# Performance work log

Measured on AMD Instinct MI355X. Metric: run time of the kernel, lower is better.

The kernel has to match this reference:

```python
import jax, jax.numpy as jnp
import numpy as np
from jax import lax

SUBSTEPS = 10
MACRO_DT = 1.0
MICRO_DT = MACRO_DT / float(SUBSTEPS)
MAX_DAYS = 4  # matches fill_max of delta_t_days; inactive batch items are masked to zero update


def _laplacian3d(u):
    # u: [B, 1, D, H, W]; 6-point stencil with zero (Dirichlet) padding at the boundary
    up = jnp.pad(u, ((0, 0), (0, 0), (1, 1), (1, 1), (1, 1)))
    return (up[:, :, 2:, 1:-1, 1:-1] + up[:, :, :-2, 1:-1, 1:-1]
            + up[:, :, 1:-1, 2:, 1:-1] + up[:, :, 1:-1, :-2, 1:-1]
            + up[:, :, 1:-1, 1:-1, 2:] + up[:, :, 1:-1, 1:-1, :-2]
            - 6.0 * u)


def _fisher_kolmogorov(u, D_map, rho_map):
    # du/dt = D * laplacian(u) + rho * u * (1 - u)
    return D_map * _laplacian3d(u) + rho_map * u * (1.0 - u)


def setup_inputs() -> dict:
    key = jax.random.key(0)
    k1, k2, k3, k4 = jax.random.split(key, 4)
    shape = (2, 1, 128, 128, 128)
    u_t0 = jax.random.uniform(k1, shape, dtype=jnp.float32)
    D_map = jax.random.uniform(k2, shape, dtype=jnp.float32) * 0.1   # diffusion, keep CFL-stable
    rho_map = jax.random.uniform(k3, shape, dtype=jnp.float32) * 0.5  # proliferation rate
    delta_t_days = jax.random.randint(k4, (2,), 0, MAX_DAYS, dtype=jnp.int32)
    return {"u_t0": u_t0, "D_map": D_map, "rho_map": rho_map, "delta_t_days": delta_t_days}


def reference(u_t0, D_map, rho_map, delta_t_days):
    # Sequential explicit-Euler rollout with per-batch-item active masking.
    days = jnp.arange(MAX_DAYS * SUBSTEPS, dtype=jnp.int32) // SUBSTEPS  # macro day of each micro-step

    def micro_step(u, day):
        active = (day < delta_t_days).astype(u.dtype)[:, None, None, None, None]  # [B,1,1,1,1]
        du_dt = _fisher_kolmogorov(u, D_map, rho_map)
        return u + active * MICRO_DT * du_dt, None

    u_final, _ = lax.scan(micro_step, u_t0, days)
    return jnp.clip(u_final, 0.0, 1.0)
```

## Files before the change

kernel.cpp:

```cpp
#include <hip/hip_runtime.h>


constexpr int NX = 128, NY = 128, NZ = 128;
constexpr int PLANE = NX * NY;
constexpr int VOL   = NZ * PLANE;
constexpr int TOTAL = 2 * VOL;
constexpr int NQ    = TOTAL / 4;
constexpr int ZB    = 4;
constexpr int NTHREADS = NQ / ZB;
constexpr int STEP_BLOCKS = NTHREADS / 256;
constexpr int CLIP_BLOCKS = NQ / 256;
constexpr float DT = 0.1f;
constexpr int MAX_STEPS = 40;

__device__ __forceinline__ float4 ld4(const float* p) {
    return *(const float4*)p;
}

__global__ __launch_bounds__(256)
void fk_step(const float* __restrict__ src, float* __restrict__ dst,
             const float* __restrict__ Dm, const float* __restrict__ Rm,
             const int* __restrict__ dtd, int t)
{
    const int tid = blockIdx.x * 256 + threadIdx.x;
    const int b   = tid >> 17;

    int d = dtd[b];
    d = d < 0 ? 0 : (d > 4 ? 4 : d);
    if (t >= d * 10) return;

    const int xq = tid & 31;
    const int y  = (tid >> 5) & (NY - 1);
    const int zb = (tid >> 12) & 31;
    const int z0 = zb * ZB;
    const int base = (b << 21) + z0 * PLANE + y * NX + (xq << 2);

    const float4 zero = make_float4(0.f, 0.f, 0.f, 0.f);

    float4 up[ZB + 2];
    #pragma unroll
    for (int j = 0; j < ZB + 2; ++j) {
        const int z = z0 - 1 + j;
        up[j] = (z >= 0 && z < NZ) ? ld4(src + base + (j - 1) * PLANE) : zero;
    }

    float4 ym[ZB], yp[ZB], Dv[ZB], Rv[ZB];
    float lft[ZB], rgt[ZB];
    const bool has_ym = (y > 0), has_yp = (y < NY - 1);
    const bool has_l = (xq > 0), has_r = (xq < 31);
    #pragma unroll
    for (int k = 0; k < ZB; ++k) {
        const int idx = base + k * PLANE;
        ym[k] = has_ym ? ld4(src + idx - NX) : zero;
        yp[k] = has_yp ? ld4(src + idx + NX) : zero;
        lft[k] = has_l ? src[idx - 1] : 0.0f;
        rgt[k] = has_r ? src[idx + 4] : 0.0f;
        Dv[k] = ld4(Dm + idx);
        Rv[k] = ld4(Rm + idx);
    }

    #pragma unroll
    for (int k = 0; k < ZB; ++k) {
        const float4 c  = up[k + 1];
        const float4 zm = up[k];
        const float4 zp = up[k + 2];
        float4 o;
        {
            const float lap = (lft[k] + c.y) + (ym[k].x + yp[k].x) + (zm.x + zp.x) - 6.0f * c.x;
            o.x = fmaf(DT, fmaf(Dv[k].x, lap, Rv[k].x * c.x * (1.0f - c.x)), c.x);
        }
        {
            const float lap = (c.x + c.z) + (ym[k].y + yp[k].y) + (zm.y + zp.y) - 6.0f * c.y;
            o.y = fmaf(DT, fmaf(Dv[k].y, lap, Rv[k].y * c.y * (1.0f - c.y)), c.y);
        }
        {
            const float lap = (c.y + c.w) + (ym[k].z + yp[k].z) + (zm.z + zp.z) - 6.0f * c.z;
            o.z = fmaf(DT, fmaf(Dv[k].z, lap, Rv[k].z * c.z * (1.0f - c.z)), c.z);
        }
        {
            const float lap = (c.z + rgt[k]) + (ym[k].w + yp[k].w) + (zm.w + zp.w) - 6.0f * c.w;
            o.w = fmaf(DT, fmaf(Dv[k].w, lap, Rv[k].w * c.w * (1.0f - c.w)), c.w);
        }
        *(float4*)(dst + base + k * PLANE) = o;
    }
}

__global__ __launch_bounds__(256)
void fk_clip(const float* __restrict__ u0, float* __restrict__ out,
             const int* __restrict__ dtd)
{
    const int i4 = blockIdx.x * 256 + threadIdx.x;
    const int b  = i4 >> 19;
    int d = dtd[b];
    d = d < 0 ? 0 : (d > 4 ? 4 : d);
    const float4 v = (d > 0) ? ((const float4*)out)[i4] : ((const float4*)u0)[i4];
    float4 o;
    o.x = fminf(fmaxf(v.x, 0.0f), 1.0f);
    o.y = fminf(fmaxf(v.y, 0.0f), 1.0f);
    o.z = fminf(fmaxf(v.z, 0.0f), 1.0f);
    o.w = fminf(fmaxf(v.w, 0.0f), 1.0f);
    ((float4*)out)[i4] = o;
}

extern "C" void kernel_launch(void* const* d_in, const int* in_sizes, int n_in,
                              void* d_out, int out_size, void* d_ws, size_t ws_size,
                              hipStream_t stream) {
    const float* u0  = (const float*)d_in[0];
    const float* Dm  = (const float*)d_in[1];
    const float* Rm  = (const float*)d_in[2];
    const int*   dtd = (const int*)d_in[3];
    float* out = (float*)d_out;
    float* ws  = (float*)d_ws;

    for (int t = 0; t < MAX_STEPS; ++t) {
        const float* src = (t == 0) ? u0 : ((t & 1) ? ws : out);
        float* dst = (t & 1) ? out : ws;
        fk_step<<<STEP_BLOCKS, 256, 0, stream>>>(src, dst, Dm, Rm, dtd, t);
    }
    fk_clip<<<CLIP_BLOCKS, 256, 0, stream>>>(u0, out, dtd);
}
```

Measured before the change: 286.3 us.

## Pack D and rho maps into bf16 pairs and fold clip into last step

Adds a pre-pass kernel that converts the diffusion and proliferation maps to bf16 and interleaves them into one 32-bit word per voxel. Each step then reads half the coefficient bytes. The separate clip kernel is removed: the clip is applied on each batch item's final step, and items with zero steps copy u0 into the output while clipping. The bf16 coefficients lose precision relative to the fp32 reference, which risks tolerance failures, and the final-step parity must land in the output buffer.

Result: faster. 275.1 us (-3.9%).

```diff
diff --git a/kernel.cpp b/kernel.cpp
--- a/kernel.cpp
+++ b/kernel.cpp
@@ -1,4 +1,5 @@
 #include <hip/hip_runtime.h>
+#include <cstdint>
 
 
 constexpr int NX = 128, NY = 128, NZ = 128;
@@ -9,31 +10,71 @@
 constexpr int ZB    = 4;
 constexpr int NTHREADS = NQ / ZB;
 constexpr int STEP_BLOCKS = NTHREADS / 256;
-constexpr int CLIP_BLOCKS = NQ / 256;
+constexpr int PACK_BLOCKS = NQ / 256;
 constexpr float DT = 0.1f;
 constexpr int MAX_STEPS = 40;
 
-__device__ __forceinline__ float4 ld4(const float* p) {
-    return *(const float4*)p;
+__device__ __forceinline__ float4 ld4(const float* p) { return *(const float4*)p; }
+
+__device__ __forceinline__ uint32_t f2bf(float f) {
+    uint32_t u = __float_as_uint(f);
+    u += 0x7fffu + ((u >> 16) & 1u);
+    return u >> 16;
 }
 
 __global__ __launch_bounds__(256)
+void fk_pack(const float* __restrict__ Dm, const float* __restrict__ Rm,
+             uint32_t* __restrict__ dr)
+{
+    const int i4  = blockIdx.x * 256 + threadIdx.x;
+    const int idx = i4 << 2;
+    const float4 Dv = ld4(Dm + idx);
+    const float4 Rv = ld4(Rm + idx);
+    uint4 o;
+    o.x = f2bf(Dv.x) | (f2bf(Rv.x) << 16);
+    o.y = f2bf(Dv.y) | (f2bf(Rv.y) << 16);
+    o.z = f2bf(Dv.z) | (f2bf(Rv.z) << 16);
+    o.w = f2bf(Dv.w) | (f2bf(Rv.w) << 16);
+    ((uint4*)dr)[i4] = o;
+}
+
+__device__ __forceinline__ float bf_lo(uint32_t p) { return __uint_as_float(p << 16); }
+__device__ __forceinline__ float bf_hi(uint32_t p) { return __uint_as_float(p & 0xffff0000u); }
+__device__ __forceinline__ float clip01(float v) { return fminf(fmaxf(v, 0.0f), 1.0f); }
+
+__global__ __launch_bounds__(256)
 void fk_step(const float* __restrict__ src, float* __restrict__ dst,
-             const float* __restrict__ Dm, const float* __restrict__ Rm,
-             const int* __restrict__ dtd, int t)
+             const uint32_t* __restrict__ dr, const int* __restrict__ dtd, int t,
+             const float* __restrict__ u0, float* __restrict__ out)
 {
     const int tid = blockIdx.x * 256 + threadIdx.x;
     const int b   = tid >> 17;
 
     int d = dtd[b];
     d = d < 0 ? 0 : (d > 4 ? 4 : d);
-    if (t >= d * 10) return;
+    const int steps = d * 10;
 
     const int xq = tid & 31;
     const int y  = (tid >> 5) & (NY - 1);
     const int zb = (tid >> 12) & 31;
     const int z0 = zb * ZB;
     const int base = (b << 21) + z0 * PLANE + y * NX + (xq << 2);
+
+    if (t >= steps) {
+        if (steps == 0 && t == 0) {
+            #pragma unroll
+            for (int k = 0; k < ZB; ++k) {
+                const int idx = base + k * PLANE;
+                const float4 v = ld4(u0 + idx);
+                float4 o;
+                o.x = clip01(v.x); o.y = clip01(v.y);
+                o.z = clip01(v.z); o.w = clip01(v.w);
+                *(float4*)(out + idx) = o;
+            }
+        }
+        return;
+    }
+    const bool last = (t == steps - 1);
 
     const float4 zero = make_float4(0.f, 0.f, 0.f, 0.f);
 
@@ -44,7 +85,8 @@
         up[j] = (z >= 0 && z < NZ) ? ld4(src + base + (j - 1) * PLANE) : zero;
     }
 
-    float4 ym[ZB], yp[ZB], Dv[ZB], Rv[ZB];
+    float4 ym[ZB], yp[ZB];
+    uint4 pr[ZB];
     float lft[ZB], rgt[ZB];
     const bool has_ym = (y > 0), has_yp = (y < NY - 1);
     const bool has_l = (xq > 0), has_r = (xq < 31);
@@ -55,8 +97,7 @@
         yp[k] = has_yp ? ld4(src + idx + NX) : zero;
         lft[k] = has_l ? src[idx - 1] : 0.0f;
         rgt[k] = has_r ? src[idx + 4] : 0.0f;
-        Dv[k] = ld4(Dm + idx);
-        Rv[k] = ld4(Rm + idx);
+        pr[k] = *(const uint4*)(dr + idx);
     }
 
     #pragma unroll
@@ -67,39 +108,26 @@
         float4 o;
         {
             const float lap = (lft[k] + c.y) + (ym[k].x + yp[k].x) + (zm.x + zp.x) - 6.0f * c.x;
-            o.x = fmaf(DT, fmaf(Dv[k].x, lap, Rv[k].x * c.x * (1.0f - c.x)), c.x);
+            o.x = fmaf(DT, fmaf(bf_lo(pr[k].x), lap, bf_hi(pr[k].x) * c.x * (1.0f - c.x)), c.x);
         }
         {
             const float lap = (c.x + c.z) + (ym[k].y + yp[k].y) + (zm.y + zp.y) - 6.0f * c.y;
-            o.y = fmaf(DT, fmaf(Dv[k].y, lap, Rv[k].y * c.y * (1.0f - c.y)), c.y);
+            o.y = fmaf(DT, fmaf(bf_lo(pr[k].y), lap, bf_hi(pr[k].y) * c.y * (1.0f - c.y)), c.y);
         }
         {
             const float lap = (c.y + c.w) + (ym[k].z + yp[k].z) + (zm.z + zp.z) - 6.0f * c.z;
-            o.z = fmaf(DT, fmaf(Dv[k].z, lap, Rv[k].z * c.z * (1.0f - c.z)), c.z);
+            o.z = fmaf(DT, fmaf(bf_lo(pr[k].z), lap, bf_hi(pr[k].z) * c.z * (1.0f - c.z)), c.z);
         }
         {
             const float lap = (c.z + rgt[k]) + (ym[k].w + yp[k].w) + (zm.w + zp.w) - 6.0f * c.w;
-            o.w = fmaf(DT, fmaf(Dv[k].w, lap, Rv[k].w * c.w * (1.0f - c.w)), c.w);
+            o.w = fmaf(DT, fmaf(bf_lo(pr[k].w), lap, bf_hi(pr[k].w) * c.w * (1.0f - c.w)), c.w);
+        }
+        if (last) {
+            o.x = clip01(o.x); o.y = clip01(o.y);
+            o.z = clip01(o.z); o.w = clip01(o.w);
         }
         *(float4*)(dst + base + k * PLANE) = o;
     }
-}
-
-__global__ __launch_bounds__(256)
-void fk_clip(const float* __restrict__ u0, float* __restrict__ out,
-             const int* __restrict__ dtd)
-{
-    const int i4 = blockIdx.x * 256 + threadIdx.x;
-    const int b  = i4 >> 19;
-    int d = dtd[b];
-    d = d < 0 ? 0 : (d > 4 ? 4 : d);
-    const float4 v = (d > 0) ? ((const float4*)out)[i4] : ((const float4*)u0)[i4];
-    float4 o;
-    o.x = fminf(fmaxf(v.x, 0.0f), 1.0f);
-    o.y = fminf(fmaxf(v.y, 0.0f), 1.0f);
-    o.z = fminf(fmaxf(v.z, 0.0f), 1.0f);
-    o.w = fminf(fmaxf(v.w, 0.0f), 1.0f);
-    ((float4*)out)[i4] = o;
 }
 
 extern "C" void kernel_launch(void* const* d_in, const int* in_sizes, int n_in,
@@ -111,11 +139,14 @@
     const int*   dtd = (const int*)d_in[3];
     float* out = (float*)d_out;
     float* ws  = (float*)d_ws;
+    float*    ping = ws;
+    uint32_t* dr   = (uint32_t*)(ws + TOTAL);
+
+    fk_pack<<<PACK_BLOCKS, 256, 0, stream>>>(Dm, Rm, dr);
 
     for (int t = 0; t < MAX_STEPS; ++t) {
-        const float* src = (t == 0) ? u0 : ((t & 1) ? ws : out);
-        float* dst = (t & 1) ? out : ws;
-        fk_step<<<STEP_BLOCKS, 256, 0, stream>>>(src, dst, Dm, Rm, dtd, t);
+        const float* src = (t == 0) ? u0 : ((t & 1) ? ping : out);
+        float* dst = (t & 1) ? out : ping;
+        fk_step<<<STEP_BLOCKS, 256, 0, stream>>>(src, dst, dr, dtd, t, u0, out);
     }
-    fk_clip<<<CLIP_BLOCKS, 256, 0, stream>>>(u0, out, dtd);
 }
```
